# Optimization experiments

Hardware: AMD Instinct MI355X
Metric: run time of the kernel (lower is better)

## Reference

```python
import jax, jax.numpy as jnp
import numpy as np

B, T, D = 2, 1024, 1024
H, HKV = 16, 8
HD = D // H           # 64
NREP = H // HKV       # 2
NLAYERS = 3
MAXKV = T * NLAYERS   # 3072
EPS = 1e-5


def setup_inputs() -> dict:
    key = jax.random.key(0)
    ks = jax.random.split(key, 8)
    # rotary tables over full accumulated-KV range
    inv_freq = 1.0 / (10000.0 ** (jnp.arange(0, HD, 2, dtype=jnp.float32) / HD))  # (HD/2,)
    t = jnp.arange(MAXKV, dtype=jnp.float32)
    freqs = jnp.outer(t, inv_freq)  # (MAXKV, HD/2)
    return {
        "x": jax.random.normal(ks[0], (B, T, D), jnp.float32),
        "cos": jnp.cos(freqs),
        "sin": jnp.sin(freqs),
        "q_w": jax.random.normal(ks[1], (NLAYERS, D, D), jnp.float32) * 0.02,
        "k_w": jax.random.normal(ks[2], (NLAYERS, D // NREP, D), jnp.float32) * 0.02,
        "v_w": jax.random.normal(ks[3], (NLAYERS, D // NREP, D), jnp.float32) * 0.02,
        "ln_w": jnp.ones((NLAYERS, D), jnp.float32),
        "lam": jax.random.normal(ks[4], (NLAYERS,), jnp.float32) * 0.1,
        "out_w": jax.random.normal(ks[5], (D, D), jnp.float32) * 0.02,
        "final_ln_w": jnp.ones((D,), jnp.float32),
        "alpha": jnp.ones((1,), jnp.float32),
    }


def rmsnorm(x, w):
    return x * jax.lax.rsqrt(jnp.mean(x * x, axis=-1, keepdims=True) + EPS) * w


def rope(x, cos, sin):
    # x: (B, L, h, HD); cos/sin: (MAXKV, HD/2); flash_attn non-interleaved rotary
    L = x.shape[1]
    c = jnp.concatenate([cos[:L], cos[:L]], axis=-1)[None, :, None, :]
    s = jnp.concatenate([sin[:L], sin[:L]], axis=-1)[None, :, None, :]
    x1, x2 = jnp.split(x, 2, axis=-1)
    rot = jnp.concatenate([-x2, x1], axis=-1)
    return x * c + rot * s


def reference(x, cos, sin, q_w, k_w, v_w, ln_w, lam, out_w, final_ln_w, alpha):
    scale = HD ** -0.5
    # lambda weights: layernorm over sigmoid of the 3 scalars (biased var, eps=1e-5)
    s = jax.nn.sigmoid(lam)
    lw = (s - s.mean()) * jax.lax.rsqrt(s.var() + EPS)
    qidx = jnp.arange(T)
    k_list, v_list = [], []
    acc = jnp.zeros_like(x)
    for i in range(NLAYERS):
        q = (x @ q_w[i].T).reshape(B, T, H, HD)
        k = (x @ k_w[i].T).reshape(B, T, HKV, HD)
        v = (x @ v_w[i].T).reshape(B, T, HKV, HD)
        k_list.append(k)
        v_list.append(v)
        K = jnp.concatenate(k_list, axis=1)  # (B, L, HKV, HD), L=(i+1)*T
        V = jnp.concatenate(v_list, axis=1)
        L = K.shape[1]
        qr = rope(q, cos, sin)
        Kr = rope(K, cos, sin)  # whole buffer re-rotated each layer, as in original
        Kr = jnp.repeat(Kr, NREP, axis=2)  # GQA expand
        Vr = jnp.repeat(V, NREP, axis=2)
        scores = jnp.einsum('bqhd,bkhd->bhqk', qr, Kr) * scale
        # flash_attn causal=True with kv_len > q_len aligns bottom-right
        mask = jnp.arange(L)[None, :] <= (qidx + (L - T))[:, None]
        scores = jnp.where(mask[None, None], scores, -jnp.inf)
        attn = jax.nn.softmax(scores, axis=-1)
        o = jnp.einsum('bhqk,bkhd->bqhd', attn, Vr).reshape(B, T, D)
        acc = acc + rmsnorm(o, ln_w[i]) * lw[i]
    out = rmsnorm(acc + alpha * x, final_ln_w)
    return out @ out_w.T
```

## Files before the change

### kernel.cpp

```cpp
#include <hip/hip_runtime.h>
#include <type_traits>
#include <utility>

typedef unsigned short u16;
typedef unsigned int u32;
typedef short short8 __attribute__((ext_vector_type(8)));
typedef short s16x4 __attribute__((ext_vector_type(4)));
typedef __bf16 bf16x8 __attribute__((ext_vector_type(8)));
typedef float floatx4 __attribute__((ext_vector_type(4)));

template <typename V, typename = void> struct MfmaTakes : std::false_type {};
template <typename V>
struct MfmaTakes<V, std::void_t<decltype(__builtin_amdgcn_mfma_f32_16x16x32_bf16(
    std::declval<V>(), std::declval<V>(), std::declval<floatx4>(), 0, 0, 0))>>
    : std::true_type {};

template <typename V>
__device__ __forceinline__ floatx4 mfma_impl(V a, V b, floatx4 c, std::true_type) {
  return __builtin_amdgcn_mfma_f32_16x16x32_bf16(a, b, c, 0, 0, 0);
}
template <typename V>
__device__ __forceinline__ floatx4 mfma_impl(V a, V b, floatx4 c, std::false_type) {
  return __builtin_amdgcn_mfma_f32_16x16x32_bf16(
      __builtin_bit_cast(bf16x8, a), __builtin_bit_cast(bf16x8, b), c, 0, 0, 0);
}
__device__ __forceinline__ floatx4 MFMA16(short8 a, short8 b, floatx4 c) {
  return mfma_impl<short8>(a, b, c, MfmaTakes<short8>{});
}

__device__ __forceinline__ floatx4 MFMAK16(s16x4 a, s16x4 b, floatx4 c) {
  return __builtin_amdgcn_mfma_f32_16x16x16bf16_1k(a, b, c, 0, 0, 0);
}

#if defined(__has_builtin)
#if __has_builtin(__builtin_amdgcn_exp2f)
#define EXP2(x) __builtin_amdgcn_exp2f(x)
#else
#define EXP2(x) exp2f(x)
#endif
#else
#define EXP2(x) exp2f(x)
#endif

__device__ __forceinline__ u16 f2bf(float f) {
  union { float f; unsigned u; } x; x.f = f;
  unsigned r = (x.u + 0x7fffu + ((x.u >> 16) & 1u)) >> 16;
  return (u16)r;
}
__device__ __forceinline__ float bf2f(u16 v) {
  union { unsigned u; float f; } x; x.u = ((unsigned)v) << 16; return x.f;
}
__device__ __forceinline__ u32 packbf(float lo, float hi) {
  return (__float_as_uint(hi) & 0xffff0000u) | (__float_as_uint(lo) >> 16);
}
__device__ __forceinline__ u32 pack2bf(float lo, float hi) {
  return ((u32)f2bf(hi) << 16) | (u32)f2bf(lo);
}

#if defined(__has_builtin)
#if __has_builtin(__builtin_amdgcn_global_load_lds)
#define HAS_GLLDS 1
#endif
#endif
__device__ __forceinline__ void stage16(const u16* g, u16* lbase, int lane) {
#ifdef HAS_GLLDS
  __builtin_amdgcn_global_load_lds(
      (__attribute__((address_space(1))) void*)(g),
      (__attribute__((address_space(3))) void*)(lbase), 16, 0, 0);
#else
  *(uint4*)(lbase + lane * 8) = *(const uint4*)g;
#endif
}

#define QSCALE 0.18033688011112042f

__global__ __launch_bounds__(256) void prep_kernel(
    const float* __restrict__ x, const float* __restrict__ qw,
    const float* __restrict__ kw, const float* __restrict__ vw,
    const float* __restrict__ outw, const float* __restrict__ lam,
    u16* __restrict__ xb, u16* __restrict__ wcat, u16* __restrict__ outwb,
    float* __restrict__ lwbuf) {
  size_t gid = (size_t)blockIdx.x * 256 + threadIdx.x;
  if (gid == 0) {
    float s0 = 1.f / (1.f + expf(-lam[0]));
    float s1 = 1.f / (1.f + expf(-lam[1]));
    float s2 = 1.f / (1.f + expf(-lam[2]));
    float mean = (s0 + s1 + s2) * (1.f / 3.f);
    float d0 = s0 - mean, d1 = s1 - mean, d2 = s2 - mean;
    float var = (d0 * d0 + d1 * d1 + d2 * d2) * (1.f / 3.f);
    float r = rsqrtf(var + 1e-5f);
    lwbuf[0] = d0 * r; lwbuf[1] = d1 * r; lwbuf[2] = d2 * r;
  }
  if (gid < 524288) {
    float4 v = ((const float4*)x)[gid];
    ushort4 o; o.x = f2bf(v.x); o.y = f2bf(v.y); o.z = f2bf(v.z); o.w = f2bf(v.w);
    ((ushort4*)xb)[gid] = o;
    return;
  }
  size_t g2 = gid - 524288;
  if (g2 < 1572864) {
    int col4 = (int)(g2 & 255);
    int n = (int)(g2 >> 8);
    int layer = n >> 11, r = n & 2047;
    const float* srcrow;
    if (r < 1024) srcrow = qw + ((size_t)(layer * 1024 + r) << 10);
    else if (r < 1536) srcrow = kw + ((size_t)(layer * 512 + (r - 1024)) << 10);
    else srcrow = vw + ((size_t)(layer * 512 + (r - 1536)) << 10);
    float4 v = ((const float4*)srcrow)[col4];
    ushort4 o; o.x = f2bf(v.x); o.y = f2bf(v.y); o.z = f2bf(v.z); o.w = f2bf(v.w);
    ((ushort4*)wcat)[g2] = o;
    return;
  }
  size_t g3 = g2 - 1572864;
  if (g3 < 262144) {
    float4 v = ((const float4*)outw)[g3];
    ushort4 o; o.x = f2bf(v.x); o.y = f2bf(v.y); o.z = f2bf(v.z); o.w = f2bf(v.w);
    ((ushort4*)outwb)[g3] = o;
  }
}

__global__ __launch_bounds__(256) void gemm_qkv(
    const u16* __restrict__ A, const u16* __restrict__ Bw,
    const float* __restrict__ cosb, const float* __restrict__ sinb,
    u16* __restrict__ qr, u16* __restrict__ kr, u16* __restrict__ vt) {
  __shared__ u16 As[128][64];
  __shared__ u16 Bs[128][64];
  const unsigned flat = blockIdx.x;
  const int bm = (flat >> 3) & 15;
  const int bn = ((flat >> 7) << 3) + (flat & 7);
  const int tid = threadIdx.x;
  const int wave = tid >> 6, lane = tid & 63;
  const int quad = lane >> 4, l16 = lane & 15;
  const int wm = wave & 1, wn = wave >> 1;
  const int srow = lane >> 3, skc = (lane & 7) * 8;
  floatx4 acc[4][4];
#pragma unroll
  for (int i = 0; i < 4; i++)
#pragma unroll
    for (int j = 0; j < 4; j++) { acc[i][j][0] = 0.f; acc[i][j][1] = 0.f; acc[i][j][2] = 0.f; acc[i][j][3] = 0.f; }
  const u16* Abase = A + (size_t)(bm * 128) * 1024;
  const u16* Bbase = Bw + (size_t)(bn * 128) * 1024;
  for (int k0 = 0; k0 < 1024; k0 += 64) {
    __syncthreads();
#pragma unroll
    for (int i = 0; i < 4; i++) {
      int ch = wave * 4 + i;
      stage16(Abase + (size_t)(ch * 8 + srow) * 1024 + k0 + skc, &As[ch * 8][0], lane);
      stage16(Bbase + (size_t)(ch * 8 + srow) * 1024 + k0 + skc, &Bs[ch * 8][0], lane);
    }
    __syncthreads();
#pragma unroll
    for (int kf = 0; kf < 2; kf++) {
      short8 af[4], bf[4];
#pragma unroll
      for (int mi = 0; mi < 4; mi++)
        af[mi] = *(const short8*)(&As[wm * 64 + mi * 16 + l16][kf * 32 + quad * 8]);
#pragma unroll
      for (int ni = 0; ni < 4; ni++)
        bf[ni] = *(const short8*)(&Bs[wn * 64 + ni * 16 + l16][kf * 32 + quad * 8]);
#pragma unroll
      for (int mi = 0; mi < 4; mi++)
#pragma unroll
        for (int ni = 0; ni < 4; ni++)
          acc[mi][ni] = MFMA16(af[mi], bf[ni], acc[mi][ni]);
    }
  }
  const int f0 = bn * 128 + wn * 64;
  const int lay = f0 >> 11;
  const int r0 = f0 & 2047;
  const int mrow0 = bm * 128 + wm * 64;
  if (r0 < 1024) {
    const int h = r0 >> 6;
#pragma unroll
    for (int mi = 0; mi < 4; mi++)
#pragma unroll
      for (int rr = 0; rr < 4; rr++) {
        int m = mrow0 + mi * 16 + quad * 4 + rr;
        int b = m >> 10, t = m & 1023;
        const float* cp = cosb + (size_t)t * 32;
        const float* sp = sinb + (size_t)t * 32;
        float c0 = cp[l16], s0 = sp[l16];
        float c1 = cp[16 + l16], s1 = sp[16 + l16];
        float x10 = acc[mi][0][rr], x20 = acc[mi][2][rr];
        float x11 = acc[mi][1][rr], x21 = acc[mi][3][rr];
        u16* row = qr + ((((size_t)lay * 2 + b) * 16 + h) * 1024 + t) * 64;
        row[l16]      = f2bf((x10 * c0 - x20 * s0) * QSCALE);
        row[16 + l16] = f2bf((x11 * c1 - x21 * s1) * QSCALE);
        row[32 + l16] = f2bf((x20 * c0 + x10 * s0) * QSCALE);
        row[48 + l16] = f2bf((x21 * c1 + x11 * s1) * QSCALE);
      }
  } else if (r0 < 1536) {
    const int hk = (r0 - 1024) >> 6;
#pragma unroll
    for (int mi = 0; mi < 4; mi++)
#pragma unroll
      for (int rr = 0; rr < 4; rr++) {
        int m = mrow0 + mi * 16 + quad * 4 + rr;
        int b = m >> 10, t = m & 1023;
        int pos = lay * 1024 + t;
        const float* cp = cosb + (size_t)pos * 32;
        const float* sp = sinb + (size_t)pos * 32;
        float c0 = cp[l16], s0 = sp[l16];
        float c1 = cp[16 + l16], s1 = sp[16 + l16];
        float x10 = acc[mi][0][rr], x20 = acc[mi][2][rr];
        float x11 = acc[mi][1][rr], x21 = acc[mi][3][rr];
        u16* row = kr + (((size_t)(b * 8 + hk)) * 3072 + pos) * 64;
        row[l16]      = f2bf(x10 * c0 - x20 * s0);
        row[16 + l16] = f2bf(x11 * c1 - x21 * s1);
        row[32 + l16] = f2bf(x20 * c0 + x10 * s0);
        row[48 + l16] = f2bf(x21 * c1 + x11 * s1);
      }
  } else {
    const int hv = (r0 - 1536) >> 6;
#pragma unroll
    for (int mi = 0; mi < 4; mi++) {
      int m0 = mrow0 + mi * 16 + quad * 4;
      int b = m0 >> 10;
      int pos0 = lay * 1024 + (m0 & 1023);
      u16* colbase = vt + ((size_t)(b * 8 + hv) * 64) * 3072 + pos0;
#pragma unroll
      for (int ni = 0; ni < 4; ni++) {
        int d = ni * 16 + l16;
        uint2 st;
        st.x = pack2bf(acc[mi][ni][0], acc[mi][ni][1]);
        st.y = pack2bf(acc[mi][ni][2], acc[mi][ni][3]);
        *(uint2*)(colbase + (size_t)d * 3072) = st;
      }
    }
  }
}

__global__ __launch_bounds__(256) void gemm_bt(
    const u16* __restrict__ A, const u16* __restrict__ Bw,
    float* __restrict__ C, int N, int K) {
  __shared__ u16 As[64][72];
  __shared__ u16 Bs[64][72];
  const int bm = blockIdx.x, bn = blockIdx.y;
  const int tid = threadIdx.x;
  const int wave = tid >> 6, lane = tid & 63;
  const int quad = lane >> 4, l16 = lane & 15;
  const int lr = tid >> 2, lc = (tid & 3) << 4;
  floatx4 acc[4];
#pragma unroll
  for (int i = 0; i < 4; i++) { acc[i][0] = 0.f; acc[i][1] = 0.f; acc[i][2] = 0.f; acc[i][3] = 0.f; }
  const u16* Arow = A + (size_t)(bm * 64 + lr) * K;
  const u16* Brow = Bw + (size_t)(bn * 64 + lr) * K;
  for (int k0 = 0; k0 < K; k0 += 64) {
    __syncthreads();
    *(uint4*)(&As[lr][lc])     = *(const uint4*)(Arow + k0 + lc);
    *(uint4*)(&As[lr][lc + 8]) = *(const uint4*)(Arow + k0 + lc + 8);
    *(uint4*)(&Bs[lr][lc])     = *(const uint4*)(Brow + k0 + lc);
    *(uint4*)(&Bs[lr][lc + 8]) = *(const uint4*)(Brow + k0 + lc + 8);
    __syncthreads();
    const int mrow = wave * 16 + l16;
    short8 a0 = *(const short8*)(&As[mrow][quad * 8]);
    short8 a1 = *(const short8*)(&As[mrow][32 + quad * 8]);
#pragma unroll
    for (int ns = 0; ns < 4; ns++) {
      short8 b0 = *(const short8*)(&Bs[ns * 16 + l16][quad * 8]);
      short8 b1 = *(const short8*)(&Bs[ns * 16 + l16][32 + quad * 8]);
      acc[ns] = MFMA16(a0, b0, acc[ns]);
      acc[ns] = MFMA16(a1, b1, acc[ns]);
    }
  }
#pragma unroll
  for (int ns = 0; ns < 4; ns++)
#pragma unroll
    for (int r = 0; r < 4; r++) {
      int row = bm * 64 + wave * 16 + quad * 4 + r;
      int col = bn * 64 + ns * 16 + l16;
      C[(size_t)row * N + col] = acc[ns][r];
    }
}

__global__ __launch_bounds__(512, 4) void attn_v9(
    const u16* __restrict__ qr, const u16* __restrict__ kr,
    const u16* __restrict__ vt, u16* __restrict__ obS,
    float* __restrict__ lbufp) {
  __shared__ __align__(16) u16 smem[9728];
  u16* KtB = smem;
  u16* VtB = smem + 4608;
  const unsigned flat = blockIdx.x;
  const int xcd = (int)(flat & 7);
  const int m = (int)(flat >> 3);
  const int qtile = m / 12;
  const int g = m - qtile * 12;
  const int pid = g * 8 + xcd;
  const int z = pid >> 4;
  const int rb = pid & 15;
  const int b = rb >> 3, j = rb & 7;
  const int lay = (z == 5) ? 0 : ((z == 0 || z == 4) ? 1 : 2);
  const int n = lay * 32 + qtile * 4 + 4;
  int kt0, kt1;
  if (lay == 0) { kt0 = 0; kt1 = n; }
  else if (lay == 1) { int hf = n >> 1; kt0 = (z == 0) ? 0 : hf; kt1 = (z == 0) ? hf : n; }
  else {
    int t1 = n / 3, t2 = (2 * n) / 3;
    kt0 = (z == 1) ? 0 : ((z == 2) ? t1 : t2);
    kt1 = (z == 1) ? t1 : ((z == 2) ? t2 : n);
  }
  const int maskkt = lay * 32 + qtile * 4;
  const int tid = threadIdx.x, wave = tid >> 6, lane = tid & 63;
  const int quad = lane >> 4, l16 = lane & 15;
  const int hw = wave >> 2, wq = wave & 3;
  const int h = j * 2 + hw;
  const int qeffbase = lay * 1024 + qtile * 128 + wq * 32;
  const u16* qpb = qr + ((((size_t)lay * 2 + b) * 16 + h) * 1024
                         + qtile * 128 + wq * 32 + l16) * 64 + quad * 8;
  short8 qf[2][2];
  qf[0][0] = *(const short8*)(qpb);
  qf[0][1] = *(const short8*)(qpb + 32);
  qf[1][0] = *(const short8*)(qpb + 1024);
  qf[1][1] = *(const short8*)(qpb + 1056);
  const s16x4 ones4 = {16256, 16256, 16256, 16256};
  floatx4 oacc[2][4];
#pragma unroll
  for (int nt = 0; nt < 2; nt++)
#pragma unroll
    for (int dt = 0; dt < 4; dt++) { oacc[nt][dt][0] = 0.f; oacc[nt][dt][1] = 0.f; oacc[nt][dt][2] = 0.f; oacc[nt][dt][3] = 0.f; }
  floatx4 lacc[2];
  lacc[0][0] = 0.f; lacc[0][1] = 0.f; lacc[0][2] = 0.f; lacc[0][3] = 0.f;
  lacc[1] = lacc[0];
  const bool isK = (tid < 256);
  const int t2i = tid & 255;
  const int ksr = t2i >> 3, ksc = (t2i & 7) * 8;
  const int vdr = t2i >> 2, vdc = (t2i & 3) * 8;
  const u16* gp = isK
      ? kr + ((size_t)(b * 8 + j) * 3072 + kt0 * 32 + ksr) * 64 + ksc
      : vt + ((size_t)(b * 8 + j) * 64 + vdr) * 3072 + kt0 * 32 + vdc;
  const size_t gstep = isK ? 2048 : 32;
  u16* ld0 = isK ? &KtB[ksr * 72 + ksc] : &VtB[vdr * 40 + vdc];
  u16* ld1 = isK ? &KtB[2304 + ksr * 72 + ksc] : &VtB[2560 + vdr * 40 + vdc];
  uint4 gA = *(const uint4*)gp;
  *(uint4*)ld0 = gA;
  gp += gstep;
  if (kt0 + 1 < kt1) gA = *(const uint4*)gp;
  for (int kt = kt0; kt < kt1; kt++) {
    const int p = (kt - kt0) & 1;
    __syncthreads();
    if (kt + 1 < kt1) {
      *(uint4*)(p ? ld0 : ld1) = gA;
      gp += gstep;
      if (kt + 2 < kt1) gA = *(const uint4*)gp;
    }
    const bool needmask = (kt >= maskkt);
    const u16* Ktp = &KtB[p * 2304];
    const u16* Vtp = &VtB[p * 2560];
    uint2 pk[2][2];
#pragma unroll
    for (int mt = 0; mt < 2; mt++) {
      short8 kfa = *(const short8*)(&Ktp[(mt * 16 + l16) * 72 + quad * 8]);
      short8 kfb = *(const short8*)(&Ktp[(mt * 16 + l16) * 72 + 32 + quad * 8]);
      const int keyb = kt * 32 + mt * 16 + quad * 4;
#pragma unroll
      for (int nt = 0; nt < 2; nt++) {
        floatx4 s; s[0] = 0.f; s[1] = 0.f; s[2] = 0.f; s[3] = 0.f;
        s = MFMA16(kfa, qf[nt][0], s);
        s = MFMA16(kfb, qf[nt][1], s);
        float p0 = EXP2(s[0]), p1 = EXP2(s[1]);
        float p2 = EXP2(s[2]), p3 = EXP2(s[3]);
        if (needmask) {
          int qpos = qeffbase + nt * 16 + l16;
          if (keyb + 0 > qpos) p0 = 0.f;
          if (keyb + 1 > qpos) p1 = 0.f;
          if (keyb + 2 > qpos) p2 = 0.f;
          if (keyb + 3 > qpos) p3 = 0.f;
        }
        pk[mt][nt].x = packbf(p0, p1);
        pk[mt][nt].y = packbf(p2, p3);
      }
    }
    s16x4 p0f0 = __builtin_bit_cast(s16x4, pk[0][0]);
    s16x4 p1f0 = __builtin_bit_cast(s16x4, pk[1][0]);
    s16x4 p0f1 = __builtin_bit_cast(s16x4, pk[0][1]);
    s16x4 p1f1 = __builtin_bit_cast(s16x4, pk[1][1]);
    lacc[0] = MFMAK16(ones4, p0f0, lacc[0]);
    lacc[0] = MFMAK16(ones4, p1f0, lacc[0]);
    lacc[1] = MFMAK16(ones4, p0f1, lacc[1]);
    lacc[1] = MFMAK16(ones4, p1f1, lacc[1]);
#pragma unroll
    for (int dt = 0; dt < 4; dt++) {
      s16x4 v0 = *(const s16x4*)(&Vtp[(dt * 16 + l16) * 40 + quad * 4]);
      s16x4 v1 = *(const s16x4*)(&Vtp[(dt * 16 + l16) * 40 + 16 + quad * 4]);
      oacc[0][dt] = MFMAK16(v0, p0f0, oacc[0][dt]);
      oacc[0][dt] = MFMAK16(v1, p1f0, oacc[0][dt]);
      oacc[1][dt] = MFMAK16(v0, p0f1, oacc[1][dt]);
      oacc[1][dt] = MFMAK16(v1, p1f1, oacc[1][dt]);
    }
  }
  __syncthreads();
  float* Pf = (float*)smem + wave * 320;
  const int tt = lane >> 2, dd = (lane & 3) << 2;
#pragma unroll
  for (int nt = 0; nt < 2; nt++) {
    int t = qtile * 128 + wq * 32 + nt * 16 + l16;
    if (quad == 0)
      lbufp[((size_t)z * 2048 + b * 1024 + t) * 16 + h] = lacc[nt][0];
    int t2 = qtile * 128 + wq * 32 + nt * 16 + tt;
    u16* orow = obS + ((size_t)(z * 2 + b) * 1024 + t2) * 1024 + h * 64 + dd;
#pragma unroll
    for (int dt = 0; dt < 4; dt++) {
      *(floatx4*)(&Pf[l16 * 20 + quad * 4]) = oacc[nt][dt];
      floatx4 val = *(const floatx4*)(&Pf[tt * 20 + dd]);
      uint2 st; st.x = pack2bf(val[0], val[1]); st.y = pack2bf(val[2], val[3]);
      *(uint2*)(orow + dt * 16) = st;
    }
  }
}

__device__ __forceinline__ float block_sum(float v, float* red) {
  v += __shfl_xor(v, 32); v += __shfl_xor(v, 16); v += __shfl_xor(v, 8);
  v += __shfl_xor(v, 4);  v += __shfl_xor(v, 2);  v += __shfl_xor(v, 1);
  __syncthreads();
  if ((threadIdx.x & 63) == 0) red[threadIdx.x >> 6] = v;
  __syncthreads();
  return red[0] + red[1] + red[2] + red[3];
}

__global__ __launch_bounds__(256) void fused_norm(
    const u16* __restrict__ obS, const float* __restrict__ lbufp,
    const float* __restrict__ x, const float* __restrict__ lnw,
    const float* __restrict__ lwbuf, const float* __restrict__ flnw,
    const float* __restrict__ alphap, u16* __restrict__ y) {
  __shared__ float red[4];
  const int row = blockIdx.x, tid = threadIdx.x;
  float a[4] = {0.f, 0.f, 0.f, 0.f};
  const int nsl[3] = {1, 2, 3};
  const int sl[3][3] = {{5, 0, 0}, {0, 4, 0}, {1, 2, 3}};
#pragma unroll
  for (int l = 0; l < 3; l++) {
    float o0 = 0.f, o1 = 0.f, o2 = 0.f, o3 = 0.f, ls = 0.f;
#pragma unroll
    for (int si = 0; si < 3; si++) {
      if (si >= nsl[l]) break;
      int z = sl[l][si];
      uint2 v = ((const uint2*)(obS + ((size_t)z * 2048 + row) * 1024))[tid];
      o0 += bf2f((u16)(v.x & 0xffff)); o1 += bf2f((u16)(v.x >> 16));
      o2 += bf2f((u16)(v.y & 0xffff)); o3 += bf2f((u16)(v.y >> 16));
      ls += lbufp[((size_t)z * 2048 + row) * 16 + (tid >> 4)];
    }
    float linv = 1.f / ls;
    float v0 = o0 * linv, v1 = o1 * linv, v2 = o2 * linv, v3 = o3 * linv;
    float ss = v0 * v0 + v1 * v1 + v2 * v2 + v3 * v3;
    ss = block_sum(ss, red);
    float rstd = rsqrtf(ss * (1.f / 1024.f) + 1e-5f);
    float lw = lwbuf[l];
    float4 w = ((const float4*)(lnw + (size_t)l * 1024))[tid];
    a[0] += v0 * rstd * w.x * lw;
    a[1] += v1 * rstd * w.y * lw;
    a[2] += v2 * rstd * w.z * lw;
    a[3] += v3 * rstd * w.w * lw;
  }
  const float aa = alphap[0];
  float4 xv = ((const float4*)(x + (size_t)row * 1024))[tid];
  float v0 = a[0] + aa * xv.x, v1 = a[1] + aa * xv.y;
  float v2 = a[2] + aa * xv.z, v3 = a[3] + aa * xv.w;
  float ss = v0 * v0 + v1 * v1 + v2 * v2 + v3 * v3;
  ss = block_sum(ss, red);
  float rstd = rsqrtf(ss * (1.f / 1024.f) + 1e-5f);
  float4 fw = ((const float4*)flnw)[tid];
  ushort4 o;
  o.x = f2bf(v0 * rstd * fw.x); o.y = f2bf(v1 * rstd * fw.y);
  o.z = f2bf(v2 * rstd * fw.z); o.w = f2bf(v3 * rstd * fw.w);
  ((ushort4*)(y + (size_t)row * 1024))[tid] = o;
}

extern "C" void kernel_launch(void* const* d_in, const int* in_sizes, int n_in,
                              void* d_out, int out_size, void* d_ws, size_t ws_size,
                              hipStream_t stream) {
  const float* x     = (const float*)d_in[0];
  const float* cosb  = (const float*)d_in[1];
  const float* sinb  = (const float*)d_in[2];
  const float* qw    = (const float*)d_in[3];
  const float* kw    = (const float*)d_in[4];
  const float* vw    = (const float*)d_in[5];
  const float* lnw   = (const float*)d_in[6];
  const float* lam   = (const float*)d_in[7];
  const float* outw  = (const float*)d_in[8];
  const float* flnw  = (const float*)d_in[9];
  const float* alphap= (const float*)d_in[10];
  float* out = (float*)d_out;
  char* ws = (char*)d_ws;
  u16*   xb    = (u16*)  (ws + 0);
  u16*   wcat  = (u16*)  (ws + 4194304);
  u16*   obS   = (u16*)  (ws + 0);
  u16*   outwb = (u16*)  (ws + 25165824);
  float* lwbuf = (float*)(ws + 27262976);
  u16*   qr    = (u16*)  (ws + 27264000);
  u16*   kr    = (u16*)  (ws + 39846912);
  u16*   vt    = (u16*)  (ws + 46138368);
  float* lbufp = (float*)(ws + 52429824);
  u16*   yb    = (u16*)  (ws + 53216256);

  prep_kernel<<<9216, 256, 0, stream>>>(x, qw, kw, vw, outw, lam, xb, wcat, outwb, lwbuf);
  gemm_qkv<<<768, 256, 0, stream>>>(xb, wcat, cosb, sinb, qr, kr, vt);
  attn_v9<<<768, 512, 0, stream>>>(qr, kr, vt, obS, lbufp);
  fused_norm<<<2048, 256, 0, stream>>>(obS, lbufp, x, lnw, lwbuf, flnw, alphap, yb);
  gemm_bt<<<dim3(32, 16), 256, 0, stream>>>(yb, outwb, out, 1024, 1024);
}
```

Baseline: 252.5 us.

## Double attention KV tile to 64 keys and raise MFMA priority

The attention kernel now stages 64 keys per iteration instead of 32, with each thread loading two 16-byte chunks of K and V into larger double-buffered LDS tiles. This halves the number of barrier-separated iterations and spreads the fixed cost of load and sync over more MFMA work. The PV MFMA section is wrapped in s_setprio to favour matrix issue. The occupancy hint in launch bounds is dropped and LDS use roughly doubles, which may lower waves per CU and changes how the split-K work is divided.

```diff
diff --git a/kernel.cpp b/kernel.cpp
--- a/kernel.cpp
+++ b/kernel.cpp
@@ -273,13 +273,13 @@
     }
 }
 
-__global__ __launch_bounds__(512, 4) void attn_v9(
+__global__ __launch_bounds__(512) void attn_v12(
     const u16* __restrict__ qr, const u16* __restrict__ kr,
     const u16* __restrict__ vt, u16* __restrict__ obS,
     float* __restrict__ lbufp) {
-  __shared__ __align__(16) u16 smem[9728];
+  __shared__ __align__(16) u16 smem[18432];
   u16* KtB = smem;
-  u16* VtB = smem + 4608;
+  u16* VtB = smem + 9216;
   const unsigned flat = blockIdx.x;
   const int xcd = (int)(flat & 7);
   const int m = (int)(flat >> 3);
@@ -290,16 +290,16 @@
   const int rb = pid & 15;
   const int b = rb >> 3, j = rb & 7;
   const int lay = (z == 5) ? 0 : ((z == 0 || z == 4) ? 1 : 2);
-  const int n = lay * 32 + qtile * 4 + 4;
+  const int n64 = lay * 16 + qtile * 2 + 2;
   int kt0, kt1;
-  if (lay == 0) { kt0 = 0; kt1 = n; }
-  else if (lay == 1) { int hf = n >> 1; kt0 = (z == 0) ? 0 : hf; kt1 = (z == 0) ? hf : n; }
+  if (lay == 0) { kt0 = 0; kt1 = n64; }
+  else if (lay == 1) { int hf = n64 >> 1; kt0 = (z == 0) ? 0 : hf; kt1 = (z == 0) ? hf : n64; }
   else {
-    int t1 = n / 3, t2 = (2 * n) / 3;
+    int t1 = n64 / 3, t2 = (2 * n64) / 3;
     kt0 = (z == 1) ? 0 : ((z == 2) ? t1 : t2);
-    kt1 = (z == 1) ? t1 : ((z == 2) ? t2 : n);
-  }
-  const int maskkt = lay * 32 + qtile * 4;
+    kt1 = (z == 1) ? t1 : ((z == 2) ? t2 : n64);
+  }
+  const int maskkt = lay * 16 + qtile * 2;
   const int tid = threadIdx.x, wave = tid >> 6, lane = tid & 63;
   const int quad = lane >> 4, l16 = lane & 15;
   const int hw = wave >> 2, wq = wave & 3;
@@ -323,69 +323,77 @@
   lacc[1] = lacc[0];
   const bool isK = (tid < 256);
   const int t2i = tid & 255;
-  const int ksr = t2i >> 3, ksc = (t2i & 7) * 8;
-  const int vdr = t2i >> 2, vdc = (t2i & 3) * 8;
+  const int sr = t2i >> 2, sc = (t2i & 3) * 8;
   const u16* gp = isK
-      ? kr + ((size_t)(b * 8 + j) * 3072 + kt0 * 32 + ksr) * 64 + ksc
-      : vt + ((size_t)(b * 8 + j) * 64 + vdr) * 3072 + kt0 * 32 + vdc;
-  const size_t gstep = isK ? 2048 : 32;
-  u16* ld0 = isK ? &KtB[ksr * 72 + ksc] : &VtB[vdr * 40 + vdc];
-  u16* ld1 = isK ? &KtB[2304 + ksr * 72 + ksc] : &VtB[2560 + vdr * 40 + vdc];
+      ? kr + ((size_t)(b * 8 + j) * 3072 + (size_t)kt0 * 64 + sr) * 64 + sc
+      : vt + ((size_t)(b * 8 + j) * 64 + sr) * 3072 + (size_t)kt0 * 64 + sc;
+  const size_t gstep = isK ? 4096 : 64;
+  u16* lbase = isK ? &KtB[sr * 72 + sc] : &VtB[sr * 72 + sc];
   uint4 gA = *(const uint4*)gp;
-  *(uint4*)ld0 = gA;
+  uint4 gB = *(const uint4*)(gp + 32);
+  *(uint4*)(lbase)      = gA;
+  *(uint4*)(lbase + 32) = gB;
   gp += gstep;
-  if (kt0 + 1 < kt1) gA = *(const uint4*)gp;
+  if (kt0 + 1 < kt1) { gA = *(const uint4*)gp; gB = *(const uint4*)(gp + 32); }
   for (int kt = kt0; kt < kt1; kt++) {
     const int p = (kt - kt0) & 1;
     __syncthreads();
     if (kt + 1 < kt1) {
-      *(uint4*)(p ? ld0 : ld1) = gA;
+      u16* lb1 = lbase + (p ? 0 : 4608);
+      *(uint4*)(lb1)      = gA;
+      *(uint4*)(lb1 + 32) = gB;
       gp += gstep;
-      if (kt + 2 < kt1) gA = *(const uint4*)gp;
+      if (kt + 2 < kt1) { gA = *(const uint4*)gp; gB = *(const uint4*)(gp + 32); }
     }
     const bool needmask = (kt >= maskkt);
-    const u16* Ktp = &KtB[p * 2304];
-    const u16* Vtp = &VtB[p * 2560];
-    uint2 pk[2][2];
-#pragma unroll
-    for (int mt = 0; mt < 2; mt++) {
-      short8 kfa = *(const short8*)(&Ktp[(mt * 16 + l16) * 72 + quad * 8]);
-      short8 kfb = *(const short8*)(&Ktp[(mt * 16 + l16) * 72 + 32 + quad * 8]);
-      const int keyb = kt * 32 + mt * 16 + quad * 4;
-#pragma unroll
-      for (int nt = 0; nt < 2; nt++) {
-        floatx4 s; s[0] = 0.f; s[1] = 0.f; s[2] = 0.f; s[3] = 0.f;
-        s = MFMA16(kfa, qf[nt][0], s);
-        s = MFMA16(kfb, qf[nt][1], s);
-        float p0 = EXP2(s[0]), p1 = EXP2(s[1]);
-        float p2 = EXP2(s[2]), p3 = EXP2(s[3]);
-        if (needmask) {
-          int qpos = qeffbase + nt * 16 + l16;
-          if (keyb + 0 > qpos) p0 = 0.f;
-          if (keyb + 1 > qpos) p1 = 0.f;
-          if (keyb + 2 > qpos) p2 = 0.f;
-          if (keyb + 3 > qpos) p3 = 0.f;
+    const u16* Ktp = &KtB[p * 4608];
+    const u16* Vtp = &VtB[p * 4608];
+#pragma unroll
+    for (int mp = 0; mp < 2; mp++) {
+      uint2 pk[2][2];
+#pragma unroll
+      for (int mh = 0; mh < 2; mh++) {
+        const int mt = mp * 2 + mh;
+        short8 kfa = *(const short8*)(&Ktp[(mt * 16 + l16) * 72 + quad * 8]);
+        short8 kfb = *(const short8*)(&Ktp[(mt * 16 + l16) * 72 + 32 + quad * 8]);
+        const int keyb = kt * 64 + mt * 16 + quad * 4;
+#pragma unroll
+        for (int nt = 0; nt < 2; nt++) {
+          floatx4 s; s[0] = 0.f; s[1] = 0.f; s[2] = 0.f; s[3] = 0.f;
+          s = MFMA16(kfa, qf[nt][0], s);
+          s = MFMA16(kfb, qf[nt][1], s);
+          float p0 = EXP2(s[0]), p1 = EXP2(s[1]);
+          float p2 = EXP2(s[2]), p3 = EXP2(s[3]);
+          if (needmask) {
+            int qpos = qeffbase + nt * 16 + l16;
+            if (keyb + 0 > qpos) p0 = 0.f;
+            if (keyb + 1 > qpos) p1 = 0.f;
+            if (keyb + 2 > qpos) p2 = 0.f;
+            if (keyb + 3 > qpos) p3 = 0.f;
+          }
+          pk[mh][nt].x = packbf(p0, p1);
+          pk[mh][nt].y = packbf(p2, p3);
         }
-        pk[mt][nt].x = packbf(p0, p1);
-        pk[mt][nt].y = packbf(p2, p3);
       }
-    }
-    s16x4 p0f0 = __builtin_bit_cast(s16x4, pk[0][0]);
-    s16x4 p1f0 = __builtin_bit_cast(s16x4, pk[1][0]);
-    s16x4 p0f1 = __builtin_bit_cast(s16x4, pk[0][1]);
-    s16x4 p1f1 = __builtin_bit_cast(s16x4, pk[1][1]);
-    lacc[0] = MFMAK16(ones4, p0f0, lacc[0]);
-    lacc[0] = MFMAK16(ones4, p1f0, lacc[0]);
-    lacc[1] = MFMAK16(ones4, p0f1, lacc[1]);
-    lacc[1] = MFMAK16(ones4, p1f1, lacc[1]);
-#pragma unroll
-    for (int dt = 0; dt < 4; dt++) {
-      s16x4 v0 = *(const s16x4*)(&Vtp[(dt * 16 + l16) * 40 + quad * 4]);
-      s16x4 v1 = *(const s16x4*)(&Vtp[(dt * 16 + l16) * 40 + 16 + quad * 4]);
-      oacc[0][dt] = MFMAK16(v0, p0f0, oacc[0][dt]);
-      oacc[0][dt] = MFMAK16(v1, p1f0, oacc[0][dt]);
-      oacc[1][dt] = MFMAK16(v0, p0f1, oacc[1][dt]);
-      oacc[1][dt] = MFMAK16(v1, p1f1, oacc[1][dt]);
+      s16x4 p0f0 = __builtin_bit_cast(s16x4, pk[0][0]);
+      s16x4 p1f0 = __builtin_bit_cast(s16x4, pk[1][0]);
+      s16x4 p0f1 = __builtin_bit_cast(s16x4, pk[0][1]);
+      s16x4 p1f1 = __builtin_bit_cast(s16x4, pk[1][1]);
+      __builtin_amdgcn_s_setprio(1);
+      lacc[0] = MFMAK16(ones4, p0f0, lacc[0]);
+      lacc[0] = MFMAK16(ones4, p1f0, lacc[0]);
+      lacc[1] = MFMAK16(ones4, p0f1, lacc[1]);
+      lacc[1] = MFMAK16(ones4, p1f1, lacc[1]);
+#pragma unroll
+      for (int dt = 0; dt < 4; dt++) {
+        s16x4 v0 = *(const s16x4*)(&Vtp[(dt * 16 + l16) * 72 + mp * 32 + quad * 4]);
+        s16x4 v1 = *(const s16x4*)(&Vtp[(dt * 16 + l16) * 72 + mp * 32 + 16 + quad * 4]);
+        oacc[0][dt] = MFMAK16(v0, p0f0, oacc[0][dt]);
+        oacc[0][dt] = MFMAK16(v1, p1f0, oacc[0][dt]);
+        oacc[1][dt] = MFMAK16(v0, p0f1, oacc[1][dt]);
+        oacc[1][dt] = MFMAK16(v1, p1f1, oacc[1][dt]);
+      }
+      __builtin_amdgcn_s_setprio(0);
     }
   }
   __syncthreads();
@@ -494,7 +502,7 @@
 
   prep_kernel<<<9216, 256, 0, stream>>>(x, qw, kw, vw, outw, lam, xb, wcat, outwb, lwbuf);
   gemm_qkv<<<768, 256, 0, stream>>>(xb, wcat, cosb, sinb, qr, kr, vt);
-  attn_v9<<<768, 512, 0, stream>>>(qr, kr, vt, obS, lbufp);
+  attn_v12<<<768, 512, 0, stream>>>(qr, kr, vt, obS, lbufp);
   fused_norm<<<2048, 256, 0, stream>>>(obS, lbufp, x, lnw, lwbuf, flnw, alphap, yb);
   gemm_bt<<<dim3(32, 16), 256, 0, stream>>>(yb, outwb, out, 1024, 1024);
 }
```

Result: no change. 248.4 us (-1.6%).

## Double-buffer output GEMM and skip fully masked key tiles per wave in attention

Applied to the files above, without the earlier changes.

The output projection GEMM now prefetches the next K tile into registers and writes it to a second LDS buffer, so only one barrier per iteration is needed and global loads overlap the MFMAs. The attention kernel computes a per-wave diagonal tile index, skips key tiles that lie fully above the causal diagonal for that wave, and applies the mask only on the diagonal tile. The launch_bounds occupancy hint is also removed, which may change register allocation and occupancy.

```diff
diff --git a/kernel.cpp b/kernel.cpp
--- a/kernel.cpp
+++ b/kernel.cpp
@@ -233,8 +233,8 @@
 __global__ __launch_bounds__(256) void gemm_bt(
     const u16* __restrict__ A, const u16* __restrict__ Bw,
     float* __restrict__ C, int N, int K) {
-  __shared__ u16 As[64][72];
-  __shared__ u16 Bs[64][72];
+  __shared__ u16 As[2][64][72];
+  __shared__ u16 Bs[2][64][72];
   const int bm = blockIdx.x, bn = blockIdx.y;
   const int tid = threadIdx.x;
   const int wave = tid >> 6, lane = tid & 63;
@@ -245,20 +245,42 @@
   for (int i = 0; i < 4; i++) { acc[i][0] = 0.f; acc[i][1] = 0.f; acc[i][2] = 0.f; acc[i][3] = 0.f; }
   const u16* Arow = A + (size_t)(bm * 64 + lr) * K;
   const u16* Brow = Bw + (size_t)(bn * 64 + lr) * K;
-  for (int k0 = 0; k0 < K; k0 += 64) {
+  uint4 ra0 = *(const uint4*)(Arow + lc);
+  uint4 ra1 = *(const uint4*)(Arow + lc + 8);
+  uint4 rb0 = *(const uint4*)(Brow + lc);
+  uint4 rb1 = *(const uint4*)(Brow + lc + 8);
+  *(uint4*)(&As[0][lr][lc])     = ra0;
+  *(uint4*)(&As[0][lr][lc + 8]) = ra1;
+  *(uint4*)(&Bs[0][lr][lc])     = rb0;
+  *(uint4*)(&Bs[0][lr][lc + 8]) = rb1;
+  if (64 < K) {
+    ra0 = *(const uint4*)(Arow + 64 + lc);
+    ra1 = *(const uint4*)(Arow + 64 + lc + 8);
+    rb0 = *(const uint4*)(Brow + 64 + lc);
+    rb1 = *(const uint4*)(Brow + 64 + lc + 8);
+  }
+  int p = 0;
+  for (int k0 = 0; k0 < K; k0 += 64, p ^= 1) {
     __syncthreads();
-    *(uint4*)(&As[lr][lc])     = *(const uint4*)(Arow + k0 + lc);
-    *(uint4*)(&As[lr][lc + 8]) = *(const uint4*)(Arow + k0 + lc + 8);
-    *(uint4*)(&Bs[lr][lc])     = *(const uint4*)(Brow + k0 + lc);
-    *(uint4*)(&Bs[lr][lc + 8]) = *(const uint4*)(Brow + k0 + lc + 8);
-    __syncthreads();
+    if (k0 + 64 < K) {
+      *(uint4*)(&As[p ^ 1][lr][lc])     = ra0;
+      *(uint4*)(&As[p ^ 1][lr][lc + 8]) = ra1;
+      *(uint4*)(&Bs[p ^ 1][lr][lc])     = rb0;
+      *(uint4*)(&Bs[p ^ 1][lr][lc + 8]) = rb1;
+      if (k0 + 128 < K) {
+        ra0 = *(const uint4*)(Arow + k0 + 128 + lc);
+        ra1 = *(const uint4*)(Arow + k0 + 128 + lc + 8);
+        rb0 = *(const uint4*)(Brow + k0 + 128 + lc);
+        rb1 = *(const uint4*)(Brow + k0 + 128 + lc + 8);
+      }
+    }
     const int mrow = wave * 16 + l16;
-    short8 a0 = *(const short8*)(&As[mrow][quad * 8]);
-    short8 a1 = *(const short8*)(&As[mrow][32 + quad * 8]);
+    short8 a0 = *(const short8*)(&As[p][mrow][quad * 8]);
+    short8 a1 = *(const short8*)(&As[p][mrow][32 + quad * 8]);
 #pragma unroll
     for (int ns = 0; ns < 4; ns++) {
-      short8 b0 = *(const short8*)(&Bs[ns * 16 + l16][quad * 8]);
-      short8 b1 = *(const short8*)(&Bs[ns * 16 + l16][32 + quad * 8]);
+      short8 b0 = *(const short8*)(&Bs[p][ns * 16 + l16][quad * 8]);
+      short8 b1 = *(const short8*)(&Bs[p][ns * 16 + l16][32 + quad * 8]);
       acc[ns] = MFMA16(a0, b0, acc[ns]);
       acc[ns] = MFMA16(a1, b1, acc[ns]);
     }
@@ -273,7 +295,7 @@
     }
 }
 
-__global__ __launch_bounds__(512, 4) void attn_v9(
+__global__ __launch_bounds__(512) void attn_v14(
     const u16* __restrict__ qr, const u16* __restrict__ kr,
     const u16* __restrict__ vt, u16* __restrict__ obS,
     float* __restrict__ lbufp) {
@@ -299,12 +321,12 @@
     kt0 = (z == 1) ? 0 : ((z == 2) ? t1 : t2);
     kt1 = (z == 1) ? t1 : ((z == 2) ? t2 : n);
   }
-  const int maskkt = lay * 32 + qtile * 4;
   const int tid = threadIdx.x, wave = tid >> 6, lane = tid & 63;
   const int quad = lane >> 4, l16 = lane & 15;
   const int hw = wave >> 2, wq = wave & 3;
   const int h = j * 2 + hw;
   const int qeffbase = lay * 1024 + qtile * 128 + wq * 32;
+  const int maskw = lay * 32 + qtile * 4 + wq;
   const u16* qpb = qr + ((((size_t)lay * 2 + b) * 16 + h) * 1024
                          + qtile * 128 + wq * 32 + l16) * 64 + quad * 8;
   short8 qf[2][2];
@@ -343,7 +365,8 @@
       gp += gstep;
       if (kt + 2 < kt1) gA = *(const uint4*)gp;
     }
-    const bool needmask = (kt >= maskkt);
+    if (kt > maskw) continue;
+    const bool needmask = (kt == maskw);
     const u16* Ktp = &KtB[p * 2304];
     const u16* Vtp = &VtB[p * 2560];
     uint2 pk[2][2];
@@ -494,7 +517,7 @@
 
   prep_kernel<<<9216, 256, 0, stream>>>(x, qw, kw, vw, outw, lam, xb, wcat, outwb, lwbuf);
   gemm_qkv<<<768, 256, 0, stream>>>(xb, wcat, cosb, sinb, qr, kr, vt);
-  attn_v9<<<768, 512, 0, stream>>>(qr, kr, vt, obS, lbufp);
+  attn_v14<<<768, 512, 0, stream>>>(qr, kr, vt, obS, lbufp);
   fused_norm<<<2048, 256, 0, stream>>>(obS, lbufp, x, lnw, lwbuf, flnw, alphap, yb);
   gemm_bt<<<dim3(32, 16), 256, 0, stream>>>(yb, outwb, out, 1024, 1024);
 }
```

Measured after the change: 245.4 us. 1.03x faster.
